# Optimization experiments

Hardware: AMD Instinct MI355X
Metric: run time of the kernel (lower is better)

The kernel has to match this reference:

```python
import jax, jax.numpy as jnp
import numpy as np


def _fake_quant(x, num_bits):
    # Per-tensor uniform min/max fake quantization with STE (straight-through).
    qmax = float(2 ** num_bits - 1)
    mn = jnp.min(x)
    mx = jnp.max(x)
    scale = (mx - mn) / qmax
    q = jnp.round((x - mn) / scale) * scale + mn
    return x + jax.lax.stop_gradient(q - x)


def _qlinear(x, W, b, num_bits):
    xq = _fake_quant(x, num_bits)
    Wq = _fake_quant(W, num_bits)
    return xq @ Wq.T + b


def setup_inputs() -> dict:
    key = jax.random.key(0)
    ks = jax.random.split(key, 7)
    B, D, H = 8192, 1024, 1024
    s = 1.0 / np.sqrt(H)
    return {
        "input": jax.random.normal(ks[0], (B, D), jnp.float32),
        "h": jax.random.normal(ks[1], (B, H), jnp.float32),
        "c": jax.random.normal(ks[2], (B, H), jnp.float32),
        "W_in": jax.random.normal(ks[3], (4 * H, D), jnp.float32) * s,
        "b_in": jax.random.normal(ks[4], (4 * H,), jnp.float32) * s,
        "W_h": jax.random.normal(ks[5], (4 * H, H), jnp.float32) * s,
        "b_h": jax.random.normal(ks[6], (4 * H,), jnp.float32) * s,
        "num_bits": 8,
        "num_bits_grad": 8,
    }


def reference(input, h, c, W_in, b_in, W_h, b_h, num_bits, num_bits_grad):
    B = input.shape[0]
    Hd = h.shape[1]
    mixed_input = _qlinear(input, W_in, b_in, num_bits).reshape(B, 4, Hd)
    mixed_hidden = _qlinear(h, W_h, b_h, num_bits).reshape(B, 4, Hd)
    gates = mixed_input + mixed_hidden  # [B, 4, H]
    i = jax.nn.sigmoid(gates[:, 0, :])
    f = jax.nn.sigmoid(gates[:, 1, :])
    g = jnp.tanh(gates[:, 2, :])
    o = jax.nn.sigmoid(gates[:, 3, :])
    c_ = f * c + i * g
    h_ = o * jnp.tanh(c_)
    return (h_, c_)
```

## Files before the change

### kernel.cpp

```cpp
#include <hip/hip_runtime.h>
#include <hip/hip_bf16.h>

typedef unsigned short u16;
typedef int i32x4 __attribute__((ext_vector_type(4)));
typedef signed char s8;

#define NB_RED 256

__global__ void k_minmax_partial(const float* __restrict__ x, const float* __restrict__ h,
                                 const float* __restrict__ wi, const float* __restrict__ wh,
                                 float* __restrict__ partials) {
    int t = blockIdx.y;
    const float* p = (t == 0) ? x : (t == 1) ? h : (t == 2) ? wi : wh;
    int n4 = ((t < 2) ? (8192 * 1024) : (4096 * 1024)) >> 2;
    float mn = 3.4e38f, mx = -3.4e38f;
    const float4* p4 = (const float4*)p;
    for (int i = blockIdx.x * blockDim.x + threadIdx.x; i < n4; i += gridDim.x * blockDim.x) {
        float4 v = p4[i];
        mn = fminf(mn, fminf(fminf(v.x, v.y), fminf(v.z, v.w)));
        mx = fmaxf(mx, fmaxf(fmaxf(v.x, v.y), fmaxf(v.z, v.w)));
    }
    for (int d = 1; d < 64; d <<= 1) {
        mn = fminf(mn, __shfl_xor(mn, d));
        mx = fmaxf(mx, __shfl_xor(mx, d));
    }
    __shared__ float smn[4], smx[4];
    int wv = threadIdx.x >> 6;
    if ((threadIdx.x & 63) == 0) { smn[wv] = mn; smx[wv] = mx; }
    __syncthreads();
    if (threadIdx.x == 0) {
        mn = fminf(fminf(smn[0], smn[1]), fminf(smn[2], smn[3]));
        mx = fmaxf(fmaxf(smx[0], smx[1]), fmaxf(smx[2], smx[3]));
        partials[(t * NB_RED + blockIdx.x) * 2 + 0] = mn;
        partials[(t * NB_RED + blockIdx.x) * 2 + 1] = mx;
    }
}

__global__ void k_minmax_final(const float* __restrict__ partials, const int* __restrict__ nbits,
                               float* __restrict__ params) {
    int t = blockIdx.x;
    int tid = threadIdx.x;
    float mn = partials[(t * NB_RED + tid) * 2 + 0];
    float mx = partials[(t * NB_RED + tid) * 2 + 1];
    for (int d = 1; d < 64; d <<= 1) {
        mn = fminf(mn, __shfl_xor(mn, d));
        mx = fmaxf(mx, __shfl_xor(mx, d));
    }
    __shared__ float smn[4], smx[4];
    int wv = tid >> 6;
    if ((tid & 63) == 0) { smn[wv] = mn; smx[wv] = mx; }
    __syncthreads();
    if (tid == 0) {
        mn = fminf(fminf(smn[0], smn[1]), fminf(smn[2], smn[3]));
        mx = fmaxf(fmaxf(smx[0], smx[1]), fmaxf(smx[2], smx[3]));
        float qmax = (float)((1u << (*nbits)) - 1u);
        params[t * 2 + 0] = mn;
        params[t * 2 + 1] = (mx - mn) / qmax;
    }
}

static __device__ __forceinline__ int block_reduce_i(int v, int tid) {
    for (int d = 1; d < 64; d <<= 1) v += __shfl_xor(v, d);
    __shared__ int sred[4];
    if ((tid & 63) == 0) sred[tid >> 6] = v;
    __syncthreads();
    return sred[0] + sred[1] + sred[2] + sred[3];
}

__global__ void k_quant(const float* __restrict__ x, const float* __restrict__ h,
                        const float* __restrict__ wi, const float* __restrict__ wh,
                        const float* __restrict__ params,
                        const float* __restrict__ b_in, const float* __restrict__ b_h,
                        s8* __restrict__ A8, s8* __restrict__ W8,
                        float* __restrict__ Rax, float* __restrict__ Rah,
                        float* __restrict__ Rbi, float* __restrict__ Rbh,
                        float* __restrict__ bc) {
    int b = blockIdx.x;
    int t = threadIdx.x;
    if (b < 16384) {
        int tsel = b >> 13;
        int row = b & 8191;
        const float* src = tsel ? h : x;
        float mn = params[tsel * 2 + 0], s = params[tsel * 2 + 1];
        float4 v = ((const float4*)(src + (size_t)row * 1024))[t];
        int k0 = (int)fminf(255.f, fmaxf(0.f, rintf((v.x - mn) / s)));
        int k1 = (int)fminf(255.f, fmaxf(0.f, rintf((v.y - mn) / s)));
        int k2 = (int)fminf(255.f, fmaxf(0.f, rintf((v.z - mn) / s)));
        int k3 = (int)fminf(255.f, fmaxf(0.f, rintf((v.w - mn) / s)));
        unsigned p = ((unsigned)((k0 - 128) & 0xff)) | ((unsigned)((k1 - 128) & 0xff) << 8) |
                     ((unsigned)((k2 - 128) & 0xff) << 16) | ((unsigned)((k3 - 128) & 0xff) << 24);
        *(unsigned*)(A8 + (size_t)row * 2048 + tsel * 1024 + t * 4) = p;
        int sum = block_reduce_i(k0 + k1 + k2 + k3 - 512, t);
        if (t == 0) (tsel ? Rah : Rax)[row] = (float)sum;
    } else if (b < 24576) {
        int bb = b - 16384;
        int tsel = bb >> 12;
        int row = bb & 4095;
        const float* src = tsel ? wh : wi;
        float mn = params[(2 + tsel) * 2 + 0], s = params[(2 + tsel) * 2 + 1];
        int g = row >> 10, j = row & 1023;
        int prow = (j >> 4) * 64 + g * 16 + (j & 15);
        float4 v = ((const float4*)(src + (size_t)row * 1024))[t];
        int k0 = (int)fminf(255.f, fmaxf(0.f, rintf((v.x - mn) / s)));
        int k1 = (int)fminf(255.f, fmaxf(0.f, rintf((v.y - mn) / s)));
        int k2 = (int)fminf(255.f, fmaxf(0.f, rintf((v.z - mn) / s)));
        int k3 = (int)fminf(255.f, fmaxf(0.f, rintf((v.w - mn) / s)));
        unsigned p = ((unsigned)((k0 - 128) & 0xff)) | ((unsigned)((k1 - 128) & 0xff) << 8) |
                     ((unsigned)((k2 - 128) & 0xff) << 16) | ((unsigned)((k3 - 128) & 0xff) << 24);
        *(unsigned*)(W8 + (size_t)prow * 2048 + tsel * 1024 + t * 4) = p;
        int sum = block_reduce_i(k0 + k1 + k2 + k3 - 512, t);
        if (t == 0) (tsel ? Rbh : Rbi)[prow] = (float)sum;
    } else {
        int n = (b - 24576) * 256 + t;
        int j = (n >> 6) * 16 + (n & 15);
        int g = (n >> 4) & 3;
        bc[n] = b_in[g * 1024 + j] + b_h[g * 1024 + j];
    }
}

__global__ __launch_bounds__(512, 2) void k_gemm_lstm(
    const s8* __restrict__ A8, const s8* __restrict__ W8,
    const float* __restrict__ params, const float* __restrict__ bc,
    const float* __restrict__ Rax, const float* __restrict__ Rah,
    const float* __restrict__ Rbi, const float* __restrict__ Rbh,
    const float* __restrict__ c_in, float* __restrict__ out) {
    __shared__ __align__(16) s8 As[4][16384];
    __shared__ __align__(16) s8 Bs[4][16384];

    const int tid = threadIdx.x;
    const int wave = tid >> 6, lane = tid & 63;
    const int wr = wave >> 2, wc = wave & 3;
    const int la = lane & 15, hi = lane >> 4;

    const int bid = blockIdx.x;
    const int xcd = bid & 7, l = bid >> 3;
    const int bx = l >> 2;
    const int by = xcd * 4 + (l & 3);
    const int bm = by * 256, bn = bx * 256;

    const int skb = (((tid & 3) ^ ((tid >> 3) & 3)) * 16);
    const int fR = (la >> 1) & 3;

    const float sa = params[1], sh = params[3], si = params[5], sw = params[7];
    const float csx = sa * si, csh = sh * sw;
    const float r = csx / csh;

    const s8* pA0 = A8 + (size_t)(bm + (tid >> 2)) * 2048 + skb;
    const s8* pA1 = pA0 + (size_t)128 * 2048;
    const s8* pB0 = W8 + (size_t)(bn + (tid >> 2)) * 2048 + skb;
    const s8* pB1 = pB0 + (size_t)128 * 2048;

    i32x4 acc[8][4];
#pragma unroll
    for (int m = 0; m < 8; m++)
#pragma unroll
        for (int n = 0; n < 4; n++) acc[m][n] = (i32x4)0;

#define STAGE(B, T)                                                                               \
    do {                                                                                          \
        __builtin_amdgcn_global_load_lds(                                                         \
            (const __attribute__((address_space(1))) void*)(pA0 + (T) * 64),                      \
            (__attribute__((address_space(3))) void*)&As[(B)][wave * 1024], 16, 0, 0);            \
        __builtin_amdgcn_global_load_lds(                                                         \
            (const __attribute__((address_space(1))) void*)(pA1 + (T) * 64),                      \
            (__attribute__((address_space(3))) void*)&As[(B)][(8 + wave) * 1024], 16, 0, 0);      \
        __builtin_amdgcn_global_load_lds(                                                         \
            (const __attribute__((address_space(1))) void*)(pB0 + (T) * 64),                      \
            (__attribute__((address_space(3))) void*)&Bs[(B)][wave * 1024], 16, 0, 0);            \
        __builtin_amdgcn_global_load_lds(                                                         \
            (const __attribute__((address_space(1))) void*)(pB1 + (T) * 64),                      \
            (__attribute__((address_space(3))) void*)&Bs[(B)][(8 + wave) * 1024], 16, 0, 0);      \
    } while (0)

#define COMPUTE(B)                                                                                \
    do {                                                                                          \
        i32x4 af[8], bf[4];                                                                       \
        _Pragma("unroll") for (int m = 0; m < 8; m++)                                             \
            af[m] = *(const i32x4*)&As[(B)][(wr * 128 + m * 16 + la) * 64 + ((hi ^ fR) * 16)];    \
        _Pragma("unroll") for (int n = 0; n < 4; n++)                                             \
            bf[n] = *(const i32x4*)&Bs[(B)][(wc * 64 + n * 16 + la) * 64 + ((hi ^ fR) * 16)];     \
        _Pragma("unroll") for (int m = 0; m < 8; m++)                                             \
            _Pragma("unroll") for (int n = 0; n < 4; n++)                                         \
                acc[m][n] = __builtin_amdgcn_mfma_i32_16x16x64_i8(af[m], bf[n], acc[m][n], 0, 0, 0); \
    } while (0)

    STAGE(0, 0);
    STAGE(1, 1);
    asm volatile("s_waitcnt vmcnt(4)" ::: "memory");
    __builtin_amdgcn_s_barrier();

#pragma unroll
    for (int t = 0; t < 32; ++t) {
        if (t < 30) STAGE((t + 2) & 3, t + 2);
        if (t == 16) {
#pragma unroll
            for (int m = 0; m < 8; m++)
#pragma unroll
                for (int n = 0; n < 4; n++)
#pragma unroll
                    for (int q = 0; q < 4; q++)
                        acc[m][n][q] = (int)rintf((float)acc[m][n][q] * r);
        }
        COMPUTE(t & 3);
        if (t < 30) { asm volatile("s_waitcnt vmcnt(4)" ::: "memory"); }
        else if (t == 30) { asm volatile("s_waitcnt vmcnt(0)" ::: "memory"); }
        if (t < 31) __builtin_amdgcn_s_barrier();
    }

#undef STAGE
#undef COMPUTE

    float mna = params[0], mnh = params[2], mni = params[4], mnw = params[6];
    float za = mna + 128.0f * sa, zi = mni + 128.0f * si;
    float zh = mnh + 128.0f * sh, zw = mnw + 128.0f * sw;
    float C0 = 1024.0f * (za * zi + zh * zw);
    float cax = sa * zi, cah = sh * zw;
    float cbx = si * za, cbh = sw * zh;

    const int nb = bn + wc * 64;
    float colt[4];
#pragma unroll
    for (int g = 0; g < 4; ++g) {
        int np = nb + g * 16 + la;
        colt[g] = bc[np] + cbx * Rbi[np] + cbh * Rbh[np] + C0;
    }
    const int ub = (nb >> 6) * 16 + la;

#pragma unroll
    for (int m = 0; m < 8; m++) {
#pragma unroll
        for (int q = 0; q < 4; q++) {
            int row = bm + wr * 128 + m * 16 + 4 * hi + q;
            float rterm = cax * Rax[row] + cah * Rah[row];
            float g0 = colt[0] + rterm + csh * (float)acc[m][0][q];
            float g1 = colt[1] + rterm + csh * (float)acc[m][1][q];
            float g2 = colt[2] + rterm + csh * (float)acc[m][2][q];
            float g3 = colt[3] + rterm + csh * (float)acc[m][3][q];
            float iv = 1.0f / (1.0f + __expf(-g0));
            float fv = 1.0f / (1.0f + __expf(-g1));
            float gv = tanhf(g2);
            float ov = 1.0f / (1.0f + __expf(-g3));
            size_t off = (size_t)row * 1024 + ub;
            float cv = c_in[off];
            float cn = fv * cv + iv * gv;
            float hn = ov * tanhf(cn);
            out[off] = hn;
            out[(size_t)8192 * 1024 + off] = cn;
        }
    }
}

extern "C" void kernel_launch(void* const* d_in, const int* in_sizes, int n_in,
                              void* d_out, int out_size, void* d_ws, size_t ws_size,
                              hipStream_t stream) {
    const float* x = (const float*)d_in[0];
    const float* h = (const float*)d_in[1];
    const float* c = (const float*)d_in[2];
    const float* wi = (const float*)d_in[3];
    const float* bi = (const float*)d_in[4];
    const float* wh = (const float*)d_in[5];
    const float* bh = (const float*)d_in[6];
    const int* nbits = (const int*)d_in[7];
    float* out = (float*)d_out;

    char* ws = (char*)d_ws;
    float* params   = (float*)ws;
    float* partials = (float*)(ws + 64);
    float* bc  = (float*)(ws + 16384);
    float* Rax = (float*)(ws + 32768);
    float* Rah = (float*)(ws + 65536);
    float* Rbi = (float*)(ws + 98304);
    float* Rbh = (float*)(ws + 114688);
    s8* A8 = (s8*)(ws + 131072);
    s8* W8 = (s8*)(ws + 131072 + (size_t)16 * 1024 * 1024);

    k_minmax_partial<<<dim3(NB_RED, 4), 256, 0, stream>>>(x, h, wi, wh, partials);
    k_minmax_final<<<4, 256, 0, stream>>>(partials, nbits, params);
    k_quant<<<24592, 256, 0, stream>>>(x, h, wi, wh, params, bi, bh,
                                       A8, W8, Rax, Rah, Rbi, Rbh, bc);
    k_gemm_lstm<<<512, 512, 0, stream>>>(A8, W8, params, bc, Rax, Rah, Rbi, Rbh, c, out);
}
```

Baseline: 140.2 us.

## Restructure int8 GEMM main loop into fine-grained interleaved load/MFMA phases

Replaces the 4-buffer per-K-step stage/compute loop with a double-buffered loop that processes two K-slices per iteration. Each slice is split into four MFMA sub-blocks, with LDS fragment reads and individual global-to-LDS loads interleaved between them. The sub-blocks are separated by barriers, and s_setprio raises wave priority around the MFMA bursts. The goal is to overlap memory traffic with matrix-core work and keep waves in lockstep, at the cost of many more barriers per iteration and a different wave-to-B-row mapping.

```diff
diff --git a/kernel.cpp b/kernel.cpp
--- a/kernel.cpp
+++ b/kernel.cpp
@@ -124,8 +124,8 @@
     const float* __restrict__ Rax, const float* __restrict__ Rah,
     const float* __restrict__ Rbi, const float* __restrict__ Rbh,
     const float* __restrict__ c_in, float* __restrict__ out) {
-    __shared__ __align__(16) s8 As[4][16384];
-    __shared__ __align__(16) s8 Bs[4][16384];
+    __shared__ __align__(16) s8 As[65536];
+    __shared__ __align__(16) s8 Bs[65536];
 
     const int tid = threadIdx.x;
     const int wave = tid >> 6, lane = tid & 63;
@@ -139,7 +139,9 @@
     const int bm = by * 256, bn = bx * 256;
 
     const int skb = (((tid & 3) ^ ((tid >> 3) & 3)) * 16);
-    const int fR = (la >> 1) & 3;
+    const int rx = ((hi ^ ((la >> 1) & 3)) * 16);
+    const int bh = wc >> 1;
+    const int br = (wc & 1) * 64 + la;
 
     const float sa = params[1], sh = params[3], si = params[5], sw = params[7];
     const float csx = sa * si, csh = sh * sw;
@@ -156,43 +158,49 @@
 #pragma unroll
         for (int n = 0; n < 4; n++) acc[m][n] = (i32x4)0;
 
-#define STAGE(B, T)                                                                               \
-    do {                                                                                          \
-        __builtin_amdgcn_global_load_lds(                                                         \
-            (const __attribute__((address_space(1))) void*)(pA0 + (T) * 64),                      \
-            (__attribute__((address_space(3))) void*)&As[(B)][wave * 1024], 16, 0, 0);            \
-        __builtin_amdgcn_global_load_lds(                                                         \
-            (const __attribute__((address_space(1))) void*)(pA1 + (T) * 64),                      \
-            (__attribute__((address_space(3))) void*)&As[(B)][(8 + wave) * 1024], 16, 0, 0);      \
-        __builtin_amdgcn_global_load_lds(                                                         \
-            (const __attribute__((address_space(1))) void*)(pB0 + (T) * 64),                      \
-            (__attribute__((address_space(3))) void*)&Bs[(B)][wave * 1024], 16, 0, 0);            \
-        __builtin_amdgcn_global_load_lds(                                                         \
-            (const __attribute__((address_space(1))) void*)(pB1 + (T) * 64),                      \
-            (__attribute__((address_space(3))) void*)&Bs[(B)][(8 + wave) * 1024], 16, 0, 0);      \
-    } while (0)
-
-#define COMPUTE(B)                                                                                \
-    do {                                                                                          \
-        i32x4 af[8], bf[4];                                                                       \
-        _Pragma("unroll") for (int m = 0; m < 8; m++)                                             \
-            af[m] = *(const i32x4*)&As[(B)][(wr * 128 + m * 16 + la) * 64 + ((hi ^ fR) * 16)];    \
-        _Pragma("unroll") for (int n = 0; n < 4; n++)                                             \
-            bf[n] = *(const i32x4*)&Bs[(B)][(wc * 64 + n * 16 + la) * 64 + ((hi ^ fR) * 16)];     \
-        _Pragma("unroll") for (int m = 0; m < 8; m++)                                             \
-            _Pragma("unroll") for (int n = 0; n < 4; n++)                                         \
-                acc[m][n] = __builtin_amdgcn_mfma_i32_16x16x64_i8(af[m], bf[n], acc[m][n], 0, 0, 0); \
-    } while (0)
-
-    STAGE(0, 0);
-    STAGE(1, 1);
-    asm volatile("s_waitcnt vmcnt(4)" ::: "memory");
-    __builtin_amdgcn_s_barrier();
-
-#pragma unroll
-    for (int t = 0; t < 32; ++t) {
-        if (t < 30) STAGE((t + 2) & 3, t + 2);
-        if (t == 16) {
+    i32x4 a[8], b[4];
+
+#define STGA(D, SL, H, TS)                                                                        \
+    __builtin_amdgcn_global_load_lds(                                                             \
+        (const __attribute__((address_space(1))) void*)(((H) ? pA1 : pA0) + (TS) * 64),           \
+        (__attribute__((address_space(3))) void*)(As + (D) * 32768 + (SL) * 16384 + (H) * 8192 + tid * 16), \
+        16, 0, 0)
+#define STGB(D, SL, H, TS)                                                                        \
+    __builtin_amdgcn_global_load_lds(                                                             \
+        (const __attribute__((address_space(1))) void*)(((H) ? pB1 : pB0) + (TS) * 64),           \
+        (__attribute__((address_space(3))) void*)(Bs + (D) * 32768 + (SL) * 16384 + (H) * 8192 + tid * 16), \
+        16, 0, 0)
+#define RDA4(D, SL, MLO)                                                                          \
+    do { _Pragma("unroll") for (int mm = 0; mm < 4; ++mm)                                         \
+        a[(MLO) + mm] = *(const i32x4*)(As + (D) * 32768 + (SL) * 16384 + wr * 8192 +             \
+                                        (((MLO) + mm) * 16 + la) * 64 + rx); } while (0)
+#define RDB2(D, SL, NLO)                                                                          \
+    do { _Pragma("unroll") for (int nn = 0; nn < 2; ++nn)                                         \
+        b[(NLO) + nn] = *(const i32x4*)(Bs + (D) * 32768 + (SL) * 16384 + bh * 8192 +             \
+                                        (br + ((NLO) + nn) * 16) * 64 + rx); } while (0)
+#define MM8(MLO, NLO)                                                                             \
+    do { _Pragma("unroll") for (int mm = 0; mm < 4; ++mm)                                         \
+        _Pragma("unroll") for (int nn = 0; nn < 2; ++nn)                                          \
+            acc[(MLO) + mm][(NLO) + nn] = __builtin_amdgcn_mfma_i32_16x16x64_i8(                  \
+                a[(MLO) + mm], b[(NLO) + nn], acc[(MLO) + mm][(NLO) + nn], 0, 0, 0); } while (0)
+#define VM4 asm volatile("s_waitcnt vmcnt(4)" ::: "memory")
+#define VM0 asm volatile("s_waitcnt vmcnt(0)" ::: "memory")
+#define LGK0 asm volatile("s_waitcnt lgkmcnt(0)" ::: "memory")
+#define BAR __builtin_amdgcn_s_barrier()
+#define PRIO1 __builtin_amdgcn_s_setprio(1)
+#define PRIO0 __builtin_amdgcn_s_setprio(0)
+
+    STGA(0, 0, 0, 0); STGA(0, 0, 1, 0); STGB(0, 0, 0, 0); STGB(0, 0, 1, 0);
+    STGA(0, 1, 0, 1); STGA(0, 1, 1, 1); STGB(0, 1, 0, 1); STGB(0, 1, 1, 1);
+    VM4;
+    BAR;
+
+#pragma unroll
+    for (int i = 0; i < 16; ++i) {
+        const int d = i & 1;
+        const int ts0 = 2 * i + 2, ts1 = 2 * i + 3;
+        const bool stg = (i < 15);
+        if (i == 8) {
 #pragma unroll
             for (int m = 0; m < 8; m++)
 #pragma unroll
@@ -201,14 +209,51 @@
                     for (int q = 0; q < 4; q++)
                         acc[m][n][q] = (int)rintf((float)acc[m][n][q] * r);
         }
-        COMPUTE(t & 3);
-        if (t < 30) { asm volatile("s_waitcnt vmcnt(4)" ::: "memory"); }
-        else if (t == 30) { asm volatile("s_waitcnt vmcnt(0)" ::: "memory"); }
-        if (t < 31) __builtin_amdgcn_s_barrier();
-    }
-
-#undef STAGE
-#undef COMPUTE
+        RDA4(d, 0, 0); RDB2(d, 0, 0);
+        if (stg) STGA(d ^ 1, 0, 0, ts0);
+        BAR; LGK0; PRIO1; MM8(0, 0); PRIO0; BAR;
+
+        RDB2(d, 0, 2);
+        if (stg) STGA(d ^ 1, 0, 1, ts0);
+        BAR; LGK0; PRIO1; MM8(0, 2); PRIO0; BAR;
+
+        RDA4(d, 0, 4);
+        if (stg) STGB(d ^ 1, 0, 0, ts0);
+        BAR; LGK0; PRIO1; MM8(4, 0); PRIO0; BAR;
+
+        if (stg) STGB(d ^ 1, 0, 1, ts0);
+        BAR; PRIO1; MM8(4, 2); PRIO0;
+        if (i < 15) { VM4; } else { VM0; }
+        BAR;
+
+        RDA4(d, 1, 0); RDB2(d, 1, 0);
+        if (stg) STGA(d ^ 1, 1, 0, ts1);
+        BAR; LGK0; PRIO1; MM8(0, 0); PRIO0; BAR;
+
+        RDB2(d, 1, 2);
+        if (stg) STGA(d ^ 1, 1, 1, ts1);
+        BAR; LGK0; PRIO1; MM8(0, 2); PRIO0; BAR;
+
+        RDA4(d, 1, 4);
+        if (stg) STGB(d ^ 1, 1, 0, ts1);
+        BAR; LGK0; PRIO1; MM8(4, 0); PRIO0; BAR;
+
+        if (stg) STGB(d ^ 1, 1, 1, ts1);
+        BAR; PRIO1; MM8(4, 2); PRIO0;
+        if (i < 15) { VM4; BAR; }
+    }
+
+#undef STGA
+#undef STGB
+#undef RDA4
+#undef RDB2
+#undef MM8
+#undef VM4
+#undef VM0
+#undef LGK0
+#undef BAR
+#undef PRIO1
+#undef PRIO0
 
     float mna = params[0], mnh = params[2], mni = params[4], mnw = params[6];
     float za = mna + 128.0f * sa, zi = mni + 128.0f * si;
```

New measurement: 151.6 us. 8.2% more time.
